# Kernel tuning notes

Measured on AMD Instinct MI355X. Metric: run time of the kernel, lower is better.

Reference implementation:

```python
import jax, jax.numpy as jnp
import numpy as np

B, L, H, D = 2, 2048, 12, 64
POLY_Q = 2.0        # from normalizer='poly_2'
NEWTON_ITERS = 6
EPS = 1e-8


def setup_inputs() -> dict:
    key = jax.random.key(0)
    kq, kk, kv = jax.random.split(key, 3)
    query = jax.random.normal(kq, (B, L, H, D), dtype=jnp.float32)
    key_t = jax.random.normal(kk, (B, L, H, D), dtype=jnp.float32)
    value = jax.random.normal(kv, (B, L, H, D), dtype=jnp.float32)
    return {"query": query, "key": key_t, "value": value}


def poly_norm(x, q=POLY_Q):
    """Replace softmax by solving sum_k 1/(-x-c)^q = 1 for c via Newton, then
    weights = 1/(-x-c)^q. x: [..., kv_len]; reductions over last axis."""
    def poly(c):
        return 1.0 / ((-x - c) ** q)
    # c0 = min(-x) - 1  ==  -max(x) - 1, guarantees (-x - c) > 0
    c = -jnp.max(x, axis=-1, keepdims=True) - 1.0
    for _ in range(NEWTON_ITERS):
        ps = jnp.sum(poly(c), axis=-1, keepdims=True)
        psd = q * jnp.sum(1.0 / ((-x - c) ** (q + 1.0)), axis=-1, keepdims=True)
        c = c - (ps - 1.0) / (psd + EPS)
    return poly(c)


def reference(query, key, value):
    depth = query.shape[-1]
    q = query / jnp.sqrt(jnp.asarray(depth, dtype=query.dtype))
    # scores: [B, H, Q, K]
    attn = jnp.einsum('bqhd,bkhd->bhqk', q, key)
    attn = poly_norm(attn, POLY_Q).astype(query.dtype)
    # out: [B, Q, H, D]
    return jnp.einsum('bhqk,bkhd->bqhd', attn, value)
```

## Files before the change

### kernel.cpp

```cpp
#include <hip/hip_runtime.h>
#include <hip/hip_bf16.h>

#define NB 2
#define NL 2048
#define NH 12
#define ND 64
#define NEWTON 6
#define WV 8
#define TPW 16

typedef __bf16 bf16x8 __attribute__((ext_vector_type(8)));
typedef float f32x4 __attribute__((ext_vector_type(4)));
typedef float f32x2 __attribute__((ext_vector_type(2)));

#define ROR_ADD(v, n)                                                         \
  (v) += __int_as_float(__builtin_amdgcn_update_dpp(                          \
      0, __float_as_int(v), 0x120 + (n), 0xF, 0xF, true))
#define ROR_MAX(v, n)                                                         \
  (v) = fmaxf((v), __int_as_float(__builtin_amdgcn_update_dpp(                \
                  0, __float_as_int(v), 0x120 + (n), 0xF, 0xF, true)))

__device__ __forceinline__ void split_bf16(float f, __bf16& hi, __bf16& lo) {
  __bf16 h = (__bf16)f;
  hi = h;
  lo = (__bf16)(f - (float)h);
}

__global__ __launch_bounds__(256) void prep(
    const float* __restrict__ kg, const float* __restrict__ vg,
    __bf16* __restrict__ kp_hi, __bf16* __restrict__ kp_lo,
    __bf16* __restrict__ vp_hi, __bf16* __restrict__ vp_lo) {
  __shared__ __align__(16) float kv[16][260];
  const int blk = blockIdx.x;
  const int isV = blk >= NB * 128 * 3;
  const int bk = isV ? blk - NB * 128 * 3 : blk;
  const int hg = bk % 3;
  const int kt = (bk / 3) & 127;
  const int b = bk / 384;
  const int t = threadIdx.x;
  const int w = t >> 6;
  const int lane = t & 63;
  const int quad = lane >> 4;
  const int l16 = lane & 15;

  const float* __restrict__ src = isV ? vg : kg;
#pragma unroll
  for (int i = 0; i < 4; ++i) {
    const int f = i * 1024 + t * 4;
    const int key = f >> 8;
    const int rem = f & 255;
    const size_t s =
        (size_t)(b * NL + kt * 16 + key) * (NH * ND) + hg * 256 + rem;
    *(f32x4*)(&kv[key][rem]) = *(const f32x4*)(src + s);
  }
  __syncthreads();

  const int h = hg * 4 + w;

  if (!isV) {
    const float* p = &kv[l16][w * 64 + quad * 8];
    f32x4 a0 = *(const f32x4*)(p);
    f32x4 a1 = *(const f32x4*)(p + 4);
    f32x4 a2 = *(const f32x4*)(p + 32);
    f32x4 a3 = *(const f32x4*)(p + 36);
    bf16x8 h0, l0, h1, l1;
#pragma unroll
    for (int j = 0; j < 4; ++j) {
      __bf16 hb, lb;
      split_bf16(a0[j], hb, lb); h0[j] = hb;     l0[j] = lb;
      split_bf16(a1[j], hb, lb); h0[4 + j] = hb; l0[4 + j] = lb;
      split_bf16(a2[j], hb, lb); h1[j] = hb;     l1[j] = lb;
      split_bf16(a3[j], hb, lb); h1[4 + j] = hb; l1[4 + j] = lb;
    }
    const size_t basek =
        ((size_t)((b * NH + h) * 128 + kt) * 2) * 512 + lane * 8;
    *(bf16x8*)(kp_hi + basek) = h0;
    *(bf16x8*)(kp_lo + basek) = l0;
    *(bf16x8*)(kp_hi + basek + 512) = h1;
    *(bf16x8*)(kp_lo + basek + 512) = l1;
  } else {
    const int halfsel = (kt >> 3) & 1;
    const int pi = (kt >> 4) * 8 + (kt & 7);
    const int q2 = quad & 1;
    const int nhalf = quad >> 1;
    const int qdst = 2 * halfsel + q2;
#pragma unroll
    for (int nn = 0; nn < 2; ++nn) {
      const int n = nhalf * 2 + nn;
      bf16x8 hv, lv;
#pragma unroll
      for (int j = 0; j < 8; ++j) {
        __bf16 hb, lb;
        split_bf16(kv[q2 * 8 + j][w * 64 + n * 16 + l16], hb, lb);
        hv[j] = hb;
        lv[j] = lb;
      }
      const size_t off =
          ((((size_t)(b * NH + h) * 64 + pi) * 4 + n) * 64 + qdst * 16 + l16) * 8;
      *(bf16x8*)(vp_hi + off) = hv;
      *(bf16x8*)(vp_lo + off) = lv;
    }
  }
}

__launch_bounds__(512, 4)
__global__ void attn_poly(const float* __restrict__ qg,
                          const __bf16* __restrict__ kp_hi,
                          const __bf16* __restrict__ kp_lo,
                          const __bf16* __restrict__ vp_hi,
                          const __bf16* __restrict__ vp_lo,
                          float* __restrict__ outg) {
  struct PW {
    union {
      float ex[16][68];
      __bf16 ws[2][16][40];
    };
  };
  __shared__ __align__(16) PW pw[WV];
  __shared__ float redmax[WV][17];
  __shared__ float redn[NEWTON][16][2];

  const int tid = threadIdx.x;
  const int w = tid >> 6;
  const int lane = tid & 63;
  const int quad = lane >> 4;
  const int l16 = lane & 15;

  const int blk = blockIdx.x;
  const int qt = blk & 127;
  const int bh = blk >> 7;
  const int h = bh % NH;
  const int b = bh / NH;
  const int qbase = qt * 16;

  bf16x8 qhi0, qlo0, qhi1, qlo1;
  {
    const float* qp = qg + ((b * NL + qbase + l16) * NH + h) * ND + quad * 8;
    f32x4 a0 = *(const f32x4*)(qp);
    f32x4 a1 = *(const f32x4*)(qp + 4);
    f32x4 a2 = *(const f32x4*)(qp + 32);
    f32x4 a3 = *(const f32x4*)(qp + 36);
#pragma unroll
    for (int j = 0; j < 4; ++j) {
      __bf16 hb, lb;
      split_bf16(a0[j] * 0.125f, hb, lb); qhi0[j] = hb;     qlo0[j] = lb;
      split_bf16(a1[j] * 0.125f, hb, lb); qhi0[4 + j] = hb; qlo0[4 + j] = lb;
      split_bf16(a2[j] * 0.125f, hb, lb); qhi1[j] = hb;     qlo1[j] = lb;
      split_bf16(a3[j] * 0.125f, hb, lb); qhi1[4 + j] = hb; qlo1[4 + j] = lb;
    }
  }

  f32x2 y[TPW][2];
  {
    const __bf16* kbh = kp_hi + (size_t)bh * 131072;
    const __bf16* kbl = kp_lo + (size_t)bh * 131072;
#pragma unroll
    for (int t = 0; t < TPW; ++t) {
      const int ktile = w + WV * t;
      const size_t o = (size_t)ktile * 1024 + lane * 8;
      bf16x8 khi0 = *(const bf16x8*)(kbh + o);
      bf16x8 khi1 = *(const bf16x8*)(kbh + o + 512);
      bf16x8 klo0 = *(const bf16x8*)(kbl + o);
      bf16x8 klo1 = *(const bf16x8*)(kbl + o + 512);
      f32x4 acc = {0.f, 0.f, 0.f, 0.f};
      acc = __builtin_amdgcn_mfma_f32_16x16x32_bf16(qhi0, khi0, acc, 0, 0, 0);
      acc = __builtin_amdgcn_mfma_f32_16x16x32_bf16(qhi1, khi1, acc, 0, 0, 0);
      acc = __builtin_amdgcn_mfma_f32_16x16x32_bf16(qhi0, klo0, acc, 0, 0, 0);
      acc = __builtin_amdgcn_mfma_f32_16x16x32_bf16(qhi1, klo1, acc, 0, 0, 0);
      acc = __builtin_amdgcn_mfma_f32_16x16x32_bf16(qlo0, khi0, acc, 0, 0, 0);
      acc = __builtin_amdgcn_mfma_f32_16x16x32_bf16(qlo1, khi1, acc, 0, 0, 0);
      y[t][0] = __builtin_shufflevector(acc, acc, 0, 1);
      y[t][1] = __builtin_shufflevector(acc, acc, 2, 3);
    }
  }

  {
    f32x2 mx2[2] = {y[0][0], y[0][1]};
#pragma unroll
    for (int t = 1; t < TPW; ++t) {
#pragma unroll
      for (int j = 0; j < 2; ++j) {
        mx2[j].x = fmaxf(mx2[j].x, y[t][j].x);
        mx2[j].y = fmaxf(mx2[j].y, y[t][j].y);
      }
    }
#pragma unroll
    for (int j = 0; j < 2; ++j) {
      ROR_MAX(mx2[j].x, 8); ROR_MAX(mx2[j].x, 4); ROR_MAX(mx2[j].x, 2); ROR_MAX(mx2[j].x, 1);
      ROR_MAX(mx2[j].y, 8); ROR_MAX(mx2[j].y, 4); ROR_MAX(mx2[j].y, 2); ROR_MAX(mx2[j].y, 1);
    }
    if (l16 < 4) {
      float v = (l16 == 0) ? mx2[0].x : (l16 == 1) ? mx2[0].y
              : (l16 == 2) ? mx2[1].x : mx2[1].y;
      redmax[w][quad * 4 + l16] = v;
    }
    if (tid < NEWTON * 16 * 2) ((float*)redn)[tid] = 0.f;
    __syncthreads();
    f32x2 negc[2];
#pragma unroll
    for (int r = 0; r < 4; ++r) {
      float m = redmax[l16 & 7][quad * 4 + r];
      ROR_MAX(m, 4); ROR_MAX(m, 2); ROR_MAX(m, 1);
      ((float*)negc)[r] = m + 1.0f;
    }
#pragma unroll
    for (int t = 0; t < TPW; ++t) {
      y[t][0] = negc[0] - y[t][0];
      y[t][1] = negc[1] - y[t][1];
    }
  }

  for (int it = 0; it < NEWTON; ++it) {
    f32x2 ps2[2] = {{0.f, 0.f}, {0.f, 0.f}};
    f32x2 psd2[2] = {{0.f, 0.f}, {0.f, 0.f}};
#pragma unroll
    for (int t = 0; t < TPW; ++t) {
#pragma unroll
      for (int j = 0; j < 2; ++j) {
        f32x2 v = y[t][j];
        float z = __builtin_amdgcn_rcpf(v.x * v.y);
        f32x2 r1 = z * __builtin_shufflevector(v, v, 1, 0);
        f32x2 r2 = r1 * r1;
        ps2[j] += r2;
        psd2[j] += r2 * r1;
      }
    }
#pragma unroll
    for (int j = 0; j < 2; ++j) {
      ROR_ADD(ps2[j].x, 8);  ROR_ADD(ps2[j].x, 4);  ROR_ADD(ps2[j].x, 2);  ROR_ADD(ps2[j].x, 1);
      ROR_ADD(ps2[j].y, 8);  ROR_ADD(ps2[j].y, 4);  ROR_ADD(ps2[j].y, 2);  ROR_ADD(ps2[j].y, 1);
      ROR_ADD(psd2[j].x, 8); ROR_ADD(psd2[j].x, 4); ROR_ADD(psd2[j].x, 2); ROR_ADD(psd2[j].x, 1);
      ROR_ADD(psd2[j].y, 8); ROR_ADD(psd2[j].y, 4); ROR_ADD(psd2[j].y, 2); ROR_ADD(psd2[j].y, 1);
    }
    if (l16 < 4) {
      float a = (l16 == 0) ? ps2[0].x : (l16 == 1) ? ps2[0].y
              : (l16 == 2) ? ps2[1].x : ps2[1].y;
      float d = (l16 == 0) ? psd2[0].x : (l16 == 1) ? psd2[0].y
              : (l16 == 2) ? psd2[1].x : psd2[1].y;
      atomicAdd(&redn[it][quad * 4 + l16][0], a);
      atomicAdd(&redn[it][quad * 4 + l16][1], d);
    }
    __syncthreads();
    f32x2 dd[2];
#pragma unroll
    for (int r = 0; r < 4; ++r) {
      const f32x2 v = *(const f32x2*)(&redn[it][quad * 4 + r][0]);
      ((float*)dd)[r] =
          (v.x - 1.0f) * __builtin_amdgcn_rcpf(2.0f * v.y + 1e-8f);
    }
#pragma unroll
    for (int t = 0; t < TPW; ++t) {
      y[t][0] += dd[0];
      y[t][1] += dd[1];
    }
  }

  f32x4 oacc[4];
#pragma unroll
  for (int n = 0; n < 4; ++n) oacc[n] = (f32x4){0.f, 0.f, 0.f, 0.f};
  const __bf16* vpbh = vp_hi + (size_t)bh * 131072;
  const __bf16* vpbl = vp_lo + (size_t)bh * 131072;

#pragma unroll
  for (int ts = 0; ts < 2; ++ts) {
    f32x2 a = y[ts][0];
    f32x2 bb = y[ts][1];
    float za = __builtin_amdgcn_rcpf(a.x * a.y);
    float zb = __builtin_amdgcn_rcpf(bb.x * bb.y);
    f32x2 ra = za * __builtin_shufflevector(a, a, 1, 0);
    f32x2 rb = zb * __builtin_shufflevector(bb, bb, 1, 0);
    f32x2 wa = ra * ra;
    f32x2 wb = rb * rb;
    pw[w].ws[0][quad * 4 + 0][ts * 16 + l16] = (__bf16)wa.x;
    pw[w].ws[0][quad * 4 + 1][ts * 16 + l16] = (__bf16)wa.y;
    pw[w].ws[0][quad * 4 + 2][ts * 16 + l16] = (__bf16)wb.x;
    pw[w].ws[0][quad * 4 + 3][ts * 16 + l16] = (__bf16)wb.y;
  }

#pragma unroll
  for (int p = 0; p < 8; ++p) {
    const size_t vo = ((size_t)(p * 8 + w) * 4) * 512 + lane * 8;
    bf16x8 bhv0 = *(const bf16x8*)(vpbh + vo);
    bf16x8 bhv1 = *(const bf16x8*)(vpbh + vo + 512);
    bf16x8 bhv2 = *(const bf16x8*)(vpbh + vo + 1024);
    bf16x8 bhv3 = *(const bf16x8*)(vpbh + vo + 1536);
    bf16x8 blv0 = *(const bf16x8*)(vpbl + vo);
    bf16x8 blv1 = *(const bf16x8*)(vpbl + vo + 512);
    bf16x8 blv2 = *(const bf16x8*)(vpbl + vo + 1024);
    bf16x8 blv3 = *(const bf16x8*)(vpbl + vo + 1536);

    asm volatile("s_waitcnt lgkmcnt(0)" ::: "memory");
    bf16x8 aw = *(const bf16x8*)(&pw[w].ws[p & 1][l16][quad * 8]);

    if (p < 7) {
#pragma unroll
      for (int ts = 0; ts < 2; ++ts) {
        const int t = 2 * (p + 1) + ts;
        f32x2 a = y[t][0];
        f32x2 bb = y[t][1];
        float za = __builtin_amdgcn_rcpf(a.x * a.y);
        float zb = __builtin_amdgcn_rcpf(bb.x * bb.y);
        f32x2 ra = za * __builtin_shufflevector(a, a, 1, 0);
        f32x2 rb = zb * __builtin_shufflevector(bb, bb, 1, 0);
        f32x2 wa = ra * ra;
        f32x2 wb = rb * rb;
        pw[w].ws[(p + 1) & 1][quad * 4 + 0][ts * 16 + l16] = (__bf16)wa.x;
        pw[w].ws[(p + 1) & 1][quad * 4 + 1][ts * 16 + l16] = (__bf16)wa.y;
        pw[w].ws[(p + 1) & 1][quad * 4 + 2][ts * 16 + l16] = (__bf16)wb.x;
        pw[w].ws[(p + 1) & 1][quad * 4 + 3][ts * 16 + l16] = (__bf16)wb.y;
      }
    }

    oacc[0] = __builtin_amdgcn_mfma_f32_16x16x32_bf16(aw, bhv0, oacc[0], 0, 0, 0);
    oacc[1] = __builtin_amdgcn_mfma_f32_16x16x32_bf16(aw, bhv1, oacc[1], 0, 0, 0);
    oacc[2] = __builtin_amdgcn_mfma_f32_16x16x32_bf16(aw, bhv2, oacc[2], 0, 0, 0);
    oacc[3] = __builtin_amdgcn_mfma_f32_16x16x32_bf16(aw, bhv3, oacc[3], 0, 0, 0);
    oacc[0] = __builtin_amdgcn_mfma_f32_16x16x32_bf16(aw, blv0, oacc[0], 0, 0, 0);
    oacc[1] = __builtin_amdgcn_mfma_f32_16x16x32_bf16(aw, blv1, oacc[1], 0, 0, 0);
    oacc[2] = __builtin_amdgcn_mfma_f32_16x16x32_bf16(aw, blv2, oacc[2], 0, 0, 0);
    oacc[3] = __builtin_amdgcn_mfma_f32_16x16x32_bf16(aw, blv3, oacc[3], 0, 0, 0);
  }

#pragma unroll
  for (int n = 0; n < 4; ++n)
#pragma unroll
    for (int r = 0; r < 4; ++r)
      pw[w].ex[quad * 4 + r][n * 16 + l16] = oacc[n][r];
  __syncthreads();
  {
    const int row = 2 * w + (lane >> 5);
    const int d = lane & 31;
    float v0 = 0.f, v1 = 0.f;
#pragma unroll
    for (int i = 0; i < WV; ++i) {
      v0 += pw[i].ex[row][d];
      v1 += pw[i].ex[row][d + 32];
    }
    const int off = ((b * NL + qbase + row) * NH + h) * ND + d;
    outg[off] = v0;
    outg[off + 32] = v1;
  }
}

extern "C" void kernel_launch(void* const* d_in, const int* in_sizes, int n_in,
                              void* d_out, int out_size, void* d_ws, size_t ws_size,
                              hipStream_t stream) {
  const float* q = (const float*)d_in[0];
  const float* k = (const float*)d_in[1];
  const float* v = (const float*)d_in[2];

  const size_t plane = (size_t)NB * NH * ND * NL;
  __bf16* kp_hi = (__bf16*)d_ws;
  __bf16* kp_lo = kp_hi + plane;
  __bf16* vp_hi = kp_lo + plane;
  __bf16* vp_lo = vp_hi + plane;

  prep<<<NB * 128 * 3 * 2, 256, 0, stream>>>(k, v, kp_hi, kp_lo, vp_hi, vp_lo);

  attn_poly<<<NB * NH * (NL / 16), 512, 0, stream>>>(
      q, kp_hi, kp_lo, vp_hi, vp_lo, (float*)d_out);
}
```

Before: 258.0 us.

## Stage full probability slab in XOR-swizzled shared memory before PV MFMA

```diff
diff --git a/kernel.cpp b/kernel.cpp
--- a/kernel.cpp
+++ b/kernel.cpp
@@ -110,13 +110,10 @@
                           const __bf16* __restrict__ vp_hi,
                           const __bf16* __restrict__ vp_lo,
                           float* __restrict__ outg) {
-  struct PW {
-    union {
-      float ex[16][68];
-      __bf16 ws[2][16][40];
-    };
-  };
-  __shared__ __align__(16) PW pw[WV];
+  __shared__ __align__(16) union ShMem {
+    __bf16 wslab[16][2048];
+    float ex[WV][16][68];
+  } sh;
   __shared__ float redmax[WV][17];
   __shared__ float redn[NEWTON][16][2];
 
@@ -220,9 +217,10 @@
         f32x2 v = y[t][j];
         float z = __builtin_amdgcn_rcpf(v.x * v.y);
         f32x2 r1 = z * __builtin_shufflevector(v, v, 1, 0);
-        f32x2 r2 = r1 * r1;
-        ps2[j] += r2;
-        psd2[j] += r2 * r1;
+        f32x2 r2;
+        asm("v_pk_mul_f32 %0, %1, %1" : "=v"(r2) : "v"(r1));
+        asm("v_pk_add_f32 %0, %0, %1" : "+v"(ps2[j]) : "v"(r2));
+        asm("v_pk_fma_f32 %0, %1, %2, %0" : "+v"(psd2[j]) : "v"(r2), "v"(r1));
       }
     }
 #pragma unroll
@@ -255,27 +253,36 @@
     }
   }
 
+  {
+    char* slab = (char*)&sh.wslab[0][0];
+#pragma unroll
+    for (int t = 0; t < TPW; ++t) {
+      f32x2 a = y[t][0];
+      f32x2 bb = y[t][1];
+      float za = __builtin_amdgcn_rcpf(a.x * a.y);
+      float zb = __builtin_amdgcn_rcpf(bb.x * bb.y);
+      f32x2 ra = za * __builtin_shufflevector(a, a, 1, 0);
+      f32x2 rb = zb * __builtin_shufflevector(bb, bb, 1, 0);
+      f32x2 wa = ra * ra;
+      f32x2 wb = rb * rb;
+      const int c2 = ((w + WV * t) * 16 + l16) * 2;
+#pragma unroll
+      for (int j = 0; j < 4; ++j) {
+        const int r = quad * 4 + j;
+        const float wv = (j == 0) ? wa.x : (j == 1) ? wa.y
+                       : (j == 2) ? wb.x : wb.y;
+        *(__bf16*)(slab + r * 4096 + (c2 ^ ((r & 7) << 4))) = (__bf16)wv;
+      }
+    }
+  }
+  __syncthreads();
+
   f32x4 oacc[4];
 #pragma unroll
   for (int n = 0; n < 4; ++n) oacc[n] = (f32x4){0.f, 0.f, 0.f, 0.f};
   const __bf16* vpbh = vp_hi + (size_t)bh * 131072;
   const __bf16* vpbl = vp_lo + (size_t)bh * 131072;
-
-#pragma unroll
-  for (int ts = 0; ts < 2; ++ts) {
-    f32x2 a = y[ts][0];
-    f32x2 bb = y[ts][1];
-    float za = __builtin_amdgcn_rcpf(a.x * a.y);
-    float zb = __builtin_amdgcn_rcpf(bb.x * bb.y);
-    f32x2 ra = za * __builtin_shufflevector(a, a, 1, 0);
-    f32x2 rb = zb * __builtin_shufflevector(bb, bb, 1, 0);
-    f32x2 wa = ra * ra;
-    f32x2 wb = rb * rb;
-    pw[w].ws[0][quad * 4 + 0][ts * 16 + l16] = (__bf16)wa.x;
-    pw[w].ws[0][quad * 4 + 1][ts * 16 + l16] = (__bf16)wa.y;
-    pw[w].ws[0][quad * 4 + 2][ts * 16 + l16] = (__bf16)wb.x;
-    pw[w].ws[0][quad * 4 + 3][ts * 16 + l16] = (__bf16)wb.y;
-  }
+  const char* slab = (const char*)&sh.wslab[0][0];
 
 #pragma unroll
   for (int p = 0; p < 8; ++p) {
@@ -289,27 +296,9 @@
     bf16x8 blv2 = *(const bf16x8*)(vpbl + vo + 1024);
     bf16x8 blv3 = *(const bf16x8*)(vpbl + vo + 1536);
 
-    asm volatile("s_waitcnt lgkmcnt(0)" ::: "memory");
-    bf16x8 aw = *(const bf16x8*)(&pw[w].ws[p & 1][l16][quad * 8]);
-
-    if (p < 7) {
-#pragma unroll
-      for (int ts = 0; ts < 2; ++ts) {
-        const int t = 2 * (p + 1) + ts;
-        f32x2 a = y[t][0];
-        f32x2 bb = y[t][1];
-        float za = __builtin_amdgcn_rcpf(a.x * a.y);
-        float zb = __builtin_amdgcn_rcpf(bb.x * bb.y);
-        f32x2 ra = za * __builtin_shufflevector(a, a, 1, 0);
-        f32x2 rb = zb * __builtin_shufflevector(bb, bb, 1, 0);
-        f32x2 wa = ra * ra;
-        f32x2 wb = rb * rb;
-        pw[w].ws[(p + 1) & 1][quad * 4 + 0][ts * 16 + l16] = (__bf16)wa.x;
-        pw[w].ws[(p + 1) & 1][quad * 4 + 1][ts * 16 + l16] = (__bf16)wa.y;
-        pw[w].ws[(p + 1) & 1][quad * 4 + 2][ts * 16 + l16] = (__bf16)wb.x;
-        pw[w].ws[(p + 1) & 1][quad * 4 + 3][ts * 16 + l16] = (__bf16)wb.y;
-      }
-    }
+    const int c2 = ((16 * p + 8 * (quad >> 1) + w) * 16 + (quad & 1) * 8) * 2;
+    bf16x8 aw =
+        *(const bf16x8*)(slab + l16 * 4096 + (c2 ^ ((l16 & 7) << 4)));
 
     oacc[0] = __builtin_amdgcn_mfma_f32_16x16x32_bf16(aw, bhv0, oacc[0], 0, 0, 0);
     oacc[1] = __builtin_amdgcn_mfma_f32_16x16x32_bf16(aw, bhv1, oacc[1], 0, 0, 0);
@@ -321,11 +310,12 @@
     oacc[3] = __builtin_amdgcn_mfma_f32_16x16x32_bf16(aw, blv3, oacc[3], 0, 0, 0);
   }
 
+  __syncthreads();
 #pragma unroll
   for (int n = 0; n < 4; ++n)
 #pragma unroll
     for (int r = 0; r < 4; ++r)
-      pw[w].ex[quad * 4 + r][n * 16 + l16] = oacc[n][r];
+      sh.ex[w][quad * 4 + r][n * 16 + l16] = oacc[n][r];
   __syncthreads();
   {
     const int row = 2 * w + (lane >> 5);
@@ -333,8 +323,8 @@
     float v0 = 0.f, v1 = 0.f;
 #pragma unroll
     for (int i = 0; i < WV; ++i) {
-      v0 += pw[i].ex[row][d];
-      v1 += pw[i].ex[row][d + 32];
+      v0 += sh.ex[i][row][d];
+      v1 += sh.ex[i][row][d + 32];
     }
     const int off = ((b * NL + qbase + row) * NH + h) * ND + d;
     outg[off] = v0;
```

After: 269.9 us. 4.6% more time.
